# Performance work log

Measured on AMD Instinct MI355X. Metric: run time of the kernel, lower is better.

Reference implementation:

```python
import jax, jax.numpy as jnp
import numpy as np

SPATIAL_SHAPES = np.array([[100, 150], [50, 75], [25, 38], [13, 19]], dtype=np.int64)


def setup_inputs() -> dict:
    key = jax.random.key(0)
    k1, k2, k3 = jax.random.split(key, 3)
    B, heads, d = 1, 8, 32
    L, P = SPATIAL_SHAPES.shape[0], 4
    n_tokens = int(SPATIAL_SHAPES.prod(axis=1).sum())  # 19947
    Q = n_tokens
    value = jax.random.normal(k1, (B, n_tokens, heads, d), dtype=jnp.float32)
    sampling_locations = jax.random.uniform(k2, (B, Q, heads, L, P, 2), dtype=jnp.float32)
    aw = jax.random.uniform(k3, (B, Q, heads, L, P), dtype=jnp.float32)
    # normalize like the real module (softmax over L*P); keeps magnitudes realistic
    attention_weights = aw / aw.sum(axis=(-2, -1), keepdims=True)
    level_start = np.concatenate([[0], np.cumsum(SPATIAL_SHAPES.prod(axis=1))[:-1]]).astype(np.int64)
    return {
        'value': value,
        'value_spatial_shapes': jnp.asarray(SPATIAL_SHAPES),
        'value_level_start_index': jnp.asarray(level_start),
        'sampling_locations': sampling_locations,
        'attention_weights': attention_weights,
        'im2col_step': 64,
    }


def _sample_level(v, loc, Hh, Ww):
    """Bilinear grid_sample (align_corners=False, zero padding).
    v:   [B, heads, Hh*Ww, D]
    loc: [B, Q, heads, P, 2] normalized in [0,1]
    returns [B, heads, Q, P, D]
    """
    B, Q, heads, P, _ = loc.shape
    D = v.shape[-1]
    # grid = 2*loc - 1; pixel coord = (grid+1)*size/2 - 0.5  ==  loc*size - 0.5
    x = loc[..., 0] * Ww - 0.5
    y = loc[..., 1] * Hh - 0.5
    x0f = jnp.floor(x)
    y0f = jnp.floor(y)
    wx1 = x - x0f
    wy1 = y - y0f
    x0 = x0f.astype(jnp.int32)
    y0 = y0f.astype(jnp.int32)

    def gather(xi, yi):
        valid = ((xi >= 0) & (xi < Ww) & (yi >= 0) & (yi < Hh)).astype(v.dtype)
        idx = jnp.clip(yi, 0, Hh - 1) * Ww + jnp.clip(xi, 0, Ww - 1)  # [B,Q,heads,P]
        idx_t = idx.transpose(0, 2, 1, 3).reshape(B, heads, Q * P, 1)
        g = jnp.take_along_axis(v, idx_t, axis=2)  # [B,heads,Q*P,D]
        g = g.reshape(B, heads, Q, P, D)
        return g, valid.transpose(0, 2, 1, 3)[..., None]

    g00, m00 = gather(x0, y0)
    g01, m01 = gather(x0 + 1, y0)
    g10, m10 = gather(x0, y0 + 1)
    g11, m11 = gather(x0 + 1, y0 + 1)
    wx1t = wx1.transpose(0, 2, 1, 3)[..., None]
    wy1t = wy1.transpose(0, 2, 1, 3)[..., None]
    wx0t = 1.0 - wx1t
    wy0t = 1.0 - wy1t
    return (g00 * m00 * (wx0t * wy0t) + g01 * m01 * (wx1t * wy0t)
            + g10 * m10 * (wx0t * wy1t) + g11 * m11 * (wx1t * wy1t))


def msda_forward(value, spatial_shapes_np, sampling_locations, attention_weights):
    B, n_tokens, heads, D = value.shape
    Q = sampling_locations.shape[1]
    areas = [int(h) * int(w) for h, w in spatial_shapes_np]
    # value per level as [B, heads, H*W, D]
    v_bhnd = value.transpose(0, 2, 1, 3)  # [B, heads, N, D]
    out = jnp.zeros((B, Q, heads, D), dtype=value.dtype)
    start = 0
    for lvl, (Hh, Ww) in enumerate(spatial_shapes_np):
        Hh, Ww = int(Hh), int(Ww)
        v_l = jax.lax.slice_in_dim(v_bhnd, start, start + Hh * Ww, axis=2)
        loc_l = sampling_locations[:, :, :, lvl]  # [B,Q,heads,P,2]
        sampled = _sample_level(v_l, loc_l, Hh, Ww)  # [B,heads,Q,P,D]
        aw_l = attention_weights[:, :, :, lvl]  # [B,Q,heads,P]
        out = out + jnp.einsum('bhqpd,bqhp->bqhd', sampled, aw_l)
        start += Hh * Ww
    return out.reshape(B, Q, heads * D)


def reference(value, value_spatial_shapes, value_level_start_index, sampling_locations, attention_weights, im2col_step):
    spatial_shapes_np = np.asarray(jax.device_get(value_spatial_shapes))
    return msda_forward(value, spatial_shapes_np, sampling_locations, attention_weights)
```

## Files before the change

### kernel.cpp

```cpp
#include <hip/hip_runtime.h>


typedef float    f32x4 __attribute__((ext_vector_type(4)));
typedef float    f32x8 __attribute__((ext_vector_type(8)));
typedef _Float16 f16x8 __attribute__((ext_vector_type(8)));

constexpr int HEADS = 8;
constexpr int DCH   = 32;
constexpr int NSP   = 16;
constexpr int NQ    = 19947;
constexpr int QPB   = 32;
constexpr int HSTR  = NQ * DCH;
constexpr int NVAL  = NQ * HEADS * DCH;

__device__ __forceinline__ void lvl_const(int l, int& W, int& H, int& S) {
    W = (l == 0) ? 150 : (l == 1) ? 75 : (l == 2) ? 38 : 19;
    H = (l == 0) ? 100 : (l == 1) ? 50 : (l == 2) ? 25 : 13;
    S = (l == 0) ? 0 : (l == 1) ? 15000 : (l == 2) ? 18750 : 19700;
}

__global__ __launch_bounds__(256)
void cvt_kernel(const float* __restrict__ value, _Float16* __restrict__ ws)
{
    const int h = blockIdx.x & 7;
    const int i = (blockIdx.x >> 3) * 256 + threadIdx.x;
    if (i >= NQ * 4) return;
    const int c8  = i & 3;
    const int tok = i >> 2;
    const float* src = value + (size_t)tok * 256 + h * 32 + c8 * 8;
    const f32x4 a = __builtin_nontemporal_load((const f32x4*)src);
    const f32x4 b = __builtin_nontemporal_load((const f32x4*)(src + 4));
    const f32x8 v = {a.x, a.y, a.z, a.w, b.x, b.y, b.z, b.w};
    *(f16x8*)(ws + (size_t)h * HSTR + (size_t)tok * 32 + c8 * 8) =
        __builtin_convertvector(v, f16x8);
}

template <bool F16>
__global__ __launch_bounds__(128)
void msda_fwd_kernel(const void* __restrict__ valuev,
                     const float* __restrict__ loc,
                     const float* __restrict__ attw,
                     float* __restrict__ out)
{
    __shared__ float s_loc[QPB][33];
    __shared__ float s_aw [QPB][17];

    const int h    = blockIdx.x & 7;
    const int qblk = blockIdx.x >> 3;
    const int q0   = qblk * QPB;
    const int t    = threadIdx.x;

#pragma unroll
    for (int it = 0; it < 2; ++it) {
        const int idx = t + it * 128;
        const int sub = idx >> 3, j = idx & 7;
        const int q = q0 + sub;
        if (q < NQ) {
            const f32x4 v = __builtin_nontemporal_load(
                (const f32x4*)(loc + ((size_t)(q * HEADS + h)) * (NSP * 2) + j * 4));
            const int l = j >> 1;
            const float fW = (l == 0) ? 150.f : (l == 1) ? 75.f : (l == 2) ? 38.f : 19.f;
            const float fH = (l == 0) ? 100.f : (l == 1) ? 50.f : (l == 2) ? 25.f : 13.f;
            s_loc[sub][j * 4 + 0] = v.x * fW - 0.5f;
            s_loc[sub][j * 4 + 1] = v.y * fH - 0.5f;
            s_loc[sub][j * 4 + 2] = v.z * fW - 0.5f;
            s_loc[sub][j * 4 + 3] = v.w * fH - 0.5f;
        }
    }
    {
        const int sub = t >> 2, j = t & 3;
        const int q = q0 + sub;
        if (q < NQ) {
            const f32x4 w = __builtin_nontemporal_load(
                (const f32x4*)(attw + ((size_t)(q * HEADS + h)) * NSP + j * 4));
            s_aw[sub][j * 4 + 0] = w.x;
            s_aw[sub][j * 4 + 1] = w.y;
            s_aw[sub][j * 4 + 2] = w.z;
            s_aw[sub][j * 4 + 3] = w.w;
        }
    }
    __syncthreads();

    const int sub = t >> 2;
    const int jj  = t & 3;
    const int q   = q0 + sub;
    if (q >= NQ) return;

    const _Float16* vf16 = (const _Float16*)valuev + (size_t)h * HSTR + jj * 8;
    const float*    vf32 = (const float*)valuev + h * DCH + jj * 8;

    auto meta = [&](int sp, f32x4& c, int& i00, int& i01, int& i10, int& i11) {
        int W, H, S;
        lvl_const(sp >> 2, W, H, S);
        const float x  = s_loc[sub][sp * 2 + 0];
        const float y  = s_loc[sub][sp * 2 + 1];
        const float aw = s_aw[sub][sp];
        const float x0f = floorf(x);
        const float y0f = floorf(y);
        const float wx1 = x - x0f;
        const float wy1 = y - y0f;
        const float wx0 = 1.f - wx1;
        const float wy0 = 1.f - wy1;
        const int x0 = (int)x0f, y0 = (int)y0f;
        const int x1 = x0 + 1,   y1 = y0 + 1;
        const float wx0m = ((unsigned)x0 < (unsigned)W) ? wx0 : 0.f;
        const float wx1m = ((unsigned)x1 < (unsigned)W) ? wx1 : 0.f;
        const float wy0m = ((unsigned)y0 < (unsigned)H) ? aw * wy0 : 0.f;
        const float wy1m = ((unsigned)y1 < (unsigned)H) ? aw * wy1 : 0.f;
        c.x = wy0m * wx0m;
        c.y = wy0m * wx1m;
        c.z = wy1m * wx0m;
        c.w = wy1m * wx1m;
        const int cx0 = max(x0, 0), cx1 = min(x1, W - 1);
        const int cy0 = max(y0, 0), cy1 = min(y1, H - 1);
        const int r0 = S + cy0 * W;
        const int r1 = S + cy1 * W;
        i00 = r0 + cx0; i01 = r0 + cx1; i10 = r1 + cx0; i11 = r1 + cx1;
    };

    f32x8 acc = {0.f, 0.f, 0.f, 0.f, 0.f, 0.f, 0.f, 0.f};

    if constexpr (F16) {
        f32x4 cc;
        int a00, a01, a10, a11;
        meta(0, cc, a00, a01, a10, a11);
        f16x8 g00 = *(const f16x8*)(vf16 + (size_t)a00 * 32);
        f16x8 g01 = *(const f16x8*)(vf16 + (size_t)a01 * 32);
        f16x8 g10 = *(const f16x8*)(vf16 + (size_t)a10 * 32);
        f16x8 g11 = *(const f16x8*)(vf16 + (size_t)a11 * 32);
#pragma unroll
        for (int sp = 0; sp < NSP; ++sp) {
            if (sp + 1 < NSP) {
                f32x4 cn;
                int b00, b01, b10, b11;
                meta(sp + 1, cn, b00, b01, b10, b11);
                const f16x8 n00 = *(const f16x8*)(vf16 + (size_t)b00 * 32);
                const f16x8 n01 = *(const f16x8*)(vf16 + (size_t)b01 * 32);
                const f16x8 n10 = *(const f16x8*)(vf16 + (size_t)b10 * 32);
                const f16x8 n11 = *(const f16x8*)(vf16 + (size_t)b11 * 32);
#pragma unroll
                for (int k = 0; k < 8; ++k) {
                    acc[k] += cc.x * (float)g00[k];
                    acc[k] += cc.y * (float)g01[k];
                    acc[k] += cc.z * (float)g10[k];
                    acc[k] += cc.w * (float)g11[k];
                }
                cc = cn; g00 = n00; g01 = n01; g10 = n10; g11 = n11;
            } else {
#pragma unroll
                for (int k = 0; k < 8; ++k) {
                    acc[k] += cc.x * (float)g00[k];
                    acc[k] += cc.y * (float)g01[k];
                    acc[k] += cc.z * (float)g10[k];
                    acc[k] += cc.w * (float)g11[k];
                }
            }
        }
    } else {
#pragma unroll
        for (int sp = 0; sp < NSP; ++sp) {
            f32x4 c;
            int i00, i01, i10, i11;
            meta(sp, c, i00, i01, i10, i11);
            const f32x4 a0 = *(const f32x4*)(vf32 + ((size_t)i00 << 8));
            const f32x4 a1 = *(const f32x4*)(vf32 + ((size_t)i00 << 8) + 4);
            const f32x4 b0 = *(const f32x4*)(vf32 + ((size_t)i01 << 8));
            const f32x4 b1 = *(const f32x4*)(vf32 + ((size_t)i01 << 8) + 4);
            const f32x4 c0 = *(const f32x4*)(vf32 + ((size_t)i10 << 8));
            const f32x4 c1 = *(const f32x4*)(vf32 + ((size_t)i10 << 8) + 4);
            const f32x4 d0 = *(const f32x4*)(vf32 + ((size_t)i11 << 8));
            const f32x4 d1 = *(const f32x4*)(vf32 + ((size_t)i11 << 8) + 4);
#pragma unroll
            for (int k = 0; k < 4; ++k) {
                acc[k]     += c.x * a0[k] + c.y * b0[k] + c.z * c0[k] + c.w * d0[k];
                acc[k + 4] += c.x * a1[k] + c.y * b1[k] + c.z * c1[k] + c.w * d1[k];
            }
        }
    }

    float* op = out + (size_t)(q * HEADS + h) * DCH + jj * 8;
    const f32x4 lo = {acc[0], acc[1], acc[2], acc[3]};
    const f32x4 hi = {acc[4], acc[5], acc[6], acc[7]};
    __builtin_nontemporal_store(lo, (f32x4*)op);
    __builtin_nontemporal_store(hi, (f32x4*)(op + 4));
}

extern "C" void kernel_launch(void* const* d_in, const int* in_sizes, int n_in,
                              void* d_out, int out_size, void* d_ws, size_t ws_size,
                              hipStream_t stream) {
    const float* value = (const float*)d_in[0];
    const float* loc   = (const float*)d_in[3];
    const float* attw  = (const float*)d_in[4];
    float* out = (float*)d_out;

    const int qblocks = (NQ + QPB - 1) / QPB;
    const int grid = qblocks * HEADS;

    const size_t f16_bytes = (size_t)NVAL * sizeof(_Float16);
    if (ws_size >= f16_bytes) {
        _Float16* ws = (_Float16*)d_ws;
        const int cgrid = ((NQ * 4 + 255) / 256) * HEADS;
        cvt_kernel<<<cgrid, 256, 0, stream>>>(value, ws);
        msda_fwd_kernel<true><<<grid, 128, 0, stream>>>(ws, loc, attw, out);
    } else {
        msda_fwd_kernel<false><<<grid, 128, 0, stream>>>(value, loc, attw, out);
    }
}
```

Baseline: 54.99 us.

## Split sampling points across two threads per channel group and reduce with shuffle

Each query/head channel group is now handled by two threads, each covering 8 of the 16 sampling points. The partial sums are combined with a cross-lane xor shuffle, and each thread stores half of the output. Blocks grow to 256 threads and the manual software prefetch of the next sample's gathers is removed. The aim is more memory-level parallelism from more concurrent gathers per query, paid for with an extra shuffle reduction and doubled thread count.

```diff
diff --git a/kernel.cpp b/kernel.cpp
--- a/kernel.cpp
+++ b/kernel.cpp
@@ -12,12 +12,6 @@
 constexpr int QPB   = 32;
 constexpr int HSTR  = NQ * DCH;
 constexpr int NVAL  = NQ * HEADS * DCH;
-
-__device__ __forceinline__ void lvl_const(int l, int& W, int& H, int& S) {
-    W = (l == 0) ? 150 : (l == 1) ? 75 : (l == 2) ? 38 : 19;
-    H = (l == 0) ? 100 : (l == 1) ? 50 : (l == 2) ? 25 : 13;
-    S = (l == 0) ? 0 : (l == 1) ? 15000 : (l == 2) ? 18750 : 19700;
-}
 
 __global__ __launch_bounds__(256)
 void cvt_kernel(const float* __restrict__ value, _Float16* __restrict__ ws)
@@ -36,7 +30,7 @@
 }
 
 template <bool F16>
-__global__ __launch_bounds__(128)
+__global__ __launch_bounds__(256)
 void msda_fwd_kernel(const void* __restrict__ valuev,
                      const float* __restrict__ loc,
                      const float* __restrict__ attw,
@@ -50,10 +44,8 @@
     const int q0   = qblk * QPB;
     const int t    = threadIdx.x;
 
-#pragma unroll
-    for (int it = 0; it < 2; ++it) {
-        const int idx = t + it * 128;
-        const int sub = idx >> 3, j = idx & 7;
+    {
+        const int sub = t >> 3, j = t & 7;
         const int q = q0 + sub;
         if (q < NQ) {
             const f32x4 v = __builtin_nontemporal_load(
@@ -67,7 +59,7 @@
             s_loc[sub][j * 4 + 3] = v.w * fH - 0.5f;
         }
     }
-    {
+    if (t < 128) {
         const int sub = t >> 2, j = t & 3;
         const int q = q0 + sub;
         if (q < NQ) {
@@ -81,17 +73,20 @@
     }
     __syncthreads();
 
-    const int sub = t >> 2;
-    const int jj  = t & 3;
-    const int q   = q0 + sub;
+    const int sub  = t >> 3;
+    const int jj   = t & 3;
+    const int half = (t >> 2) & 1;
+    const int q    = q0 + sub;
     if (q >= NQ) return;
 
     const _Float16* vf16 = (const _Float16*)valuev + (size_t)h * HSTR + jj * 8;
     const float*    vf32 = (const float*)valuev + h * DCH + jj * 8;
 
     auto meta = [&](int sp, f32x4& c, int& i00, int& i01, int& i10, int& i11) {
-        int W, H, S;
-        lvl_const(sp >> 2, W, H, S);
+        const int l = sp >> 2;
+        const int W = (l == 0) ? 150 : (l == 1) ? 75 : (l == 2) ? 38 : 19;
+        const int H = (l == 0) ? 100 : (l == 1) ? 50 : (l == 2) ? 25 : 13;
+        const int S = (l == 0) ? 0 : (l == 1) ? 15000 : (l == 2) ? 18750 : 19700;
         const float x  = s_loc[sub][sp * 2 + 0];
         const float y  = s_loc[sub][sp * 2 + 1];
         const float aw = s_aw[sub][sp];
@@ -119,49 +114,28 @@
     };
 
     f32x8 acc = {0.f, 0.f, 0.f, 0.f, 0.f, 0.f, 0.f, 0.f};
+    const int sp0 = half * 8;
 
-    if constexpr (F16) {
-        f32x4 cc;
-        int a00, a01, a10, a11;
-        meta(0, cc, a00, a01, a10, a11);
-        f16x8 g00 = *(const f16x8*)(vf16 + (size_t)a00 * 32);
-        f16x8 g01 = *(const f16x8*)(vf16 + (size_t)a01 * 32);
-        f16x8 g10 = *(const f16x8*)(vf16 + (size_t)a10 * 32);
-        f16x8 g11 = *(const f16x8*)(vf16 + (size_t)a11 * 32);
 #pragma unroll
-        for (int sp = 0; sp < NSP; ++sp) {
-            if (sp + 1 < NSP) {
-                f32x4 cn;
-                int b00, b01, b10, b11;
-                meta(sp + 1, cn, b00, b01, b10, b11);
-                const f16x8 n00 = *(const f16x8*)(vf16 + (size_t)b00 * 32);
-                const f16x8 n01 = *(const f16x8*)(vf16 + (size_t)b01 * 32);
-                const f16x8 n10 = *(const f16x8*)(vf16 + (size_t)b10 * 32);
-                const f16x8 n11 = *(const f16x8*)(vf16 + (size_t)b11 * 32);
+    for (int u = 0; u < 8; ++u) {
+        const int sp = sp0 + u;
+        f32x4 c;
+        int i00, i01, i10, i11;
+        meta(sp, c, i00, i01, i10, i11);
+
+        if constexpr (F16) {
+            const f16x8 g00 = *(const f16x8*)(vf16 + (size_t)i00 * 32);
+            const f16x8 g01 = *(const f16x8*)(vf16 + (size_t)i01 * 32);
+            const f16x8 g10 = *(const f16x8*)(vf16 + (size_t)i10 * 32);
+            const f16x8 g11 = *(const f16x8*)(vf16 + (size_t)i11 * 32);
 #pragma unroll
-                for (int k = 0; k < 8; ++k) {
-                    acc[k] += cc.x * (float)g00[k];
-                    acc[k] += cc.y * (float)g01[k];
-                    acc[k] += cc.z * (float)g10[k];
-                    acc[k] += cc.w * (float)g11[k];
-                }
-                cc = cn; g00 = n00; g01 = n01; g10 = n10; g11 = n11;
-            } else {
-#pragma unroll
-                for (int k = 0; k < 8; ++k) {
-                    acc[k] += cc.x * (float)g00[k];
-                    acc[k] += cc.y * (float)g01[k];
-                    acc[k] += cc.z * (float)g10[k];
-                    acc[k] += cc.w * (float)g11[k];
-                }
+            for (int k = 0; k < 8; ++k) {
+                acc[k] += c.x * (float)g00[k];
+                acc[k] += c.y * (float)g01[k];
+                acc[k] += c.z * (float)g10[k];
+                acc[k] += c.w * (float)g11[k];
             }
-        }
-    } else {
-#pragma unroll
-        for (int sp = 0; sp < NSP; ++sp) {
-            f32x4 c;
-            int i00, i01, i10, i11;
-            meta(sp, c, i00, i01, i10, i11);
+        } else {
             const f32x4 a0 = *(const f32x4*)(vf32 + ((size_t)i00 << 8));
             const f32x4 a1 = *(const f32x4*)(vf32 + ((size_t)i00 << 8) + 4);
             const f32x4 b0 = *(const f32x4*)(vf32 + ((size_t)i01 << 8));
@@ -178,11 +152,13 @@
         }
     }
 
-    float* op = out + (size_t)(q * HEADS + h) * DCH + jj * 8;
-    const f32x4 lo = {acc[0], acc[1], acc[2], acc[3]};
-    const f32x4 hi = {acc[4], acc[5], acc[6], acc[7]};
-    __builtin_nontemporal_store(lo, (f32x4*)op);
-    __builtin_nontemporal_store(hi, (f32x4*)(op + 4));
+#pragma unroll
+    for (int k = 0; k < 8; ++k) acc[k] += __shfl_xor(acc[k], 4);
+
+    float* op = out + (size_t)(q * HEADS + h) * DCH + jj * 8 + half * 4;
+    const f32x4 part = half ? f32x4{acc[4], acc[5], acc[6], acc[7]}
+                            : f32x4{acc[0], acc[1], acc[2], acc[3]};
+    __builtin_nontemporal_store(part, (f32x4*)op);
 }
 
 extern "C" void kernel_launch(void* const* d_in, const int* in_sizes, int n_in,
@@ -201,8 +177,8 @@
         _Float16* ws = (_Float16*)d_ws;
         const int cgrid = ((NQ * 4 + 255) / 256) * HEADS;
         cvt_kernel<<<cgrid, 256, 0, stream>>>(value, ws);
-        msda_fwd_kernel<true><<<grid, 128, 0, stream>>>(ws, loc, attw, out);
+        msda_fwd_kernel<true><<<grid, 256, 0, stream>>>(ws, loc, attw, out);
     } else {
-        msda_fwd_kernel<false><<<grid, 128, 0, stream>>>(value, loc, attw, out);
+        msda_fwd_kernel<false><<<grid, 256, 0, stream>>>(value, loc, attw, out);
     }
 }
```

New measurement: 55.05 us. Within noise of the previous version (+0.1%).
